# Kernel optimization log

Hardware: AMD Instinct MI355X
Metric: run time of the kernel (lower is better)

## Reference

```python
import jax, jax.numpy as jnp
import numpy as np

GROUP_SIZE = 128
LORA_SCALING = 32.0 / 16.0  # lora_alpha / r


def _unpack_rows(q):
    # q: int32 [n, m] -> uint4 values [n*8, m], 8 nibbles per int32 along axis 0
    shifts = (jnp.arange(8, dtype=jnp.int32) * 4)
    vals = (q[:, None, :] >> shifts[None, :, None]) & 0xF
    return vals.reshape(q.shape[0] * 8, q.shape[1])


def _unpack_cols(q):
    # q: int32 [g, m] -> uint4 values [g, m*8], 8 nibbles per int32 along axis 1
    shifts = (jnp.arange(8, dtype=jnp.int32) * 4)
    vals = (q[:, :, None] >> shifts[None, None, :]) & 0xF
    return vals.reshape(q.shape[0], q.shape[1] * 8)


def setup_inputs() -> dict:
    key = jax.random.key(0)
    ks = jax.random.split(key, 6)
    in_f, out_f, tokens, r = 4096, 11008, 64, 16
    g = in_f // GROUP_SIZE  # 32 groups
    x = jax.random.normal(ks[0], (tokens, in_f), dtype=jnp.float32)
    qweight = jax.random.randint(ks[1], (in_f // 8, out_f), jnp.iinfo(jnp.int32).min, jnp.iinfo(jnp.int32).max, dtype=jnp.int32)
    qzeros = jax.random.randint(ks[2], (g, out_f // 8), jnp.iinfo(jnp.int32).min, jnp.iinfo(jnp.int32).max, dtype=jnp.int32)
    scales = jax.random.uniform(ks[3], (g, out_f), dtype=jnp.float32) * 0.01 + 0.001
    lora_A = jax.random.normal(ks[4], (r, in_f), dtype=jnp.float32) * 0.02
    lora_B = jax.random.normal(ks[5], (out_f, r), dtype=jnp.float32) * 0.02
    return {"x": x, "qweight": qweight, "qzeros": qzeros, "scales": scales,
            "lora_A": lora_A, "lora_B": lora_B}


def reference(x, qweight, qzeros, scales, lora_A, lora_B):
    in_f = qweight.shape[0] * 8
    # --- GPTQ int4 dequant ---
    wq = _unpack_rows(qweight).astype(jnp.float32)          # [in, out]
    zeros = (_unpack_cols(qzeros) + 1).astype(jnp.float32)  # [groups, out] (GPTQ +1 offset)
    g_idx = jnp.arange(in_f) // GROUP_SIZE                  # [in]
    W = scales[g_idx] * (wq - zeros[g_idx])                 # [in, out]
    # base quantized matmul
    result = x @ W                                          # [tokens, out]
    # --- LoRA adapter (single active adapter, dropout=0, tmp_weight=1) ---
    lora_out = (x @ lora_A.T) @ lora_B.T                    # [tokens, out]
    return result + lora_out * LORA_SCALING
```

## Files before the change

kernel.cpp:

```cpp
#include <hip/hip_runtime.h>
#include <stdint.h>

#define TOKENS 64
#define IN_F   4096
#define OUT_F  11008
#define RANK   16
#define GS     128
#define NG     32
#define ZCOLS  (OUT_F / 8)
#define LORA_SCALE 2.0f

using short8  = __attribute__((ext_vector_type(8))) short;
using float4v = __attribute__((ext_vector_type(4))) float;

static __device__ inline uint16_t f2bf(float f, float* back) {
    uint32_t u = __float_as_uint(f);
    uint32_t r = (u + 0x7FFFu + ((u >> 16) & 1u)) >> 16;
    *back = __uint_as_float(r << 16);
    return (uint16_t)r;
}

static __device__ inline float dot4(float4 a, float4 b) {
    return a.x * b.x + a.y * b.y + a.z * b.z + a.w * b.w;
}

__global__ __launch_bounds__(256) void prep_kernel(
        const float* __restrict__ x,
        const float* __restrict__ loraA,
        uint4* __restrict__ xf4,
        float* __restrict__ xsumT,
        float* __restrict__ midTT) {
    __shared__ float redg[256];
    __shared__ float redm[4][16];
    const int t    = blockIdx.x;
    const int tid  = threadIdx.x;
    const int lane = tid & 63;
    const int wv   = tid >> 6;

    float4 xv[4];
    const float4* xp = (const float4*)(x + (size_t)t * IN_F + tid * 16);
    #pragma unroll
    for (int i = 0; i < 4; ++i) xv[i] = xp[i];

    union { uint16_t u[16]; uint4 q[2]; } ob;
    float s = 0.f;
    #pragma unroll
    for (int i = 0; i < 4; ++i) {
        float b;
        ob.u[i * 4 + 0] = f2bf(xv[i].x, &b); s += b;
        ob.u[i * 4 + 1] = f2bf(xv[i].y, &b); s += b;
        ob.u[i * 4 + 2] = f2bf(xv[i].z, &b); s += b;
        ob.u[i * 4 + 3] = f2bf(xv[i].w, &b); s += b;
    }
    {
        const int mm = t >> 4, nn = t & 15;
        const int kchunk = tid >> 1;
        #pragma unroll
        for (int i = 0; i < 2; ++i) {
            const int qd = (tid * 2 + i) & 3;
            xf4[(size_t)((mm * 128 + kchunk) * 64 + qd * 16 + nn)] = ob.q[i];
        }
    }
    redg[tid] = s;

    float pj[16];
    #pragma unroll
    for (int j = 0; j < 16; ++j) {
        const float4* ap = (const float4*)(loraA + (size_t)j * IN_F + tid * 16);
        float ps = 0.f;
        #pragma unroll
        for (int i = 0; i < 4; ++i) {
            float4 a = ap[i];
            ps += a.x * xv[i].x + a.y * xv[i].y + a.z * xv[i].z + a.w * xv[i].w;
        }
        pj[j] = ps;
    }
    #pragma unroll
    for (int j = 0; j < 16; ++j) {
        #pragma unroll
        for (int off = 32; off; off >>= 1) pj[j] += __shfl_down(pj[j], off);
    }
    if (lane == 0) {
        #pragma unroll
        for (int j = 0; j < 16; ++j) redm[wv][j] = pj[j];
    }
    __syncthreads();
    if (tid < NG) {
        float g = 0.f;
        #pragma unroll
        for (int i = 0; i < 8; ++i) g += redg[tid * 8 + i];
        xsumT[tid * TOKENS + t] = g;
    }
    if (tid < 16)
        midTT[t * RANK + tid] = redm[0][tid] + redm[1][tid] + redm[2][tid] + redm[3][tid];
}

#define LOADG(st, g) do {                                                       \
    _Pragma("unroll")                                                           \
    for (int mt = 0; mt < 2; ++mt)                                              \
        _Pragma("unroll")                                                       \
        for (int ks = 0; ks < 4; ++ks)                                          \
            A[st][mt * 4 + ks] =                                                \
                xf4[(size_t)(((mh * 2 + mt) * 128 + (g) * 4 + ks) * 64) + lane];\
    _Pragma("unroll")                                                           \
    for (int ks = 0; ks < 4; ++ks)                                              \
        B[st][ks] = qwc[(size_t)((g) * 16 + ks * 4 + quad) * OUT_F];            \
    _Pragma("unroll")                                                           \
    for (int mt = 0; mt < 2; ++mt)                                              \
        XS[st][mt] = *(const float4*)(xsumT + (g) * 64 +                        \
                                      (mh * 2 + mt) * 16 + quad * 4);           \
    S[st] = scales[(size_t)(g) * OUT_F + col];                                  \
    Z[st] = qz[(size_t)(g) * ZCOLS + (col >> 3)];                               \
} while (0)

#define COMPUTEG(st) do {                                                       \
    float4v accg[2];                                                            \
    accg[0] = (float4v){0.f, 0.f, 0.f, 0.f};                                    \
    accg[1] = (float4v){0.f, 0.f, 0.f, 0.f};                                    \
    _Pragma("unroll")                                                           \
    for (int ks = 0; ks < 4; ++ks) {                                            \
        union { uint4 u; short8 s; } af0, af1;                                  \
        af0.u = A[st][ks];                                                      \
        af1.u = A[st][4 + ks];                                                  \
        uint32_t q  = B[st][ks];                                                \
        uint32_t lo = q & 0x0F0F0F0Fu;                                          \
        uint32_t hi = (q >> 4) & 0x0F0F0F0Fu;                                   \
        union { uint32_t u32[4]; short8 s8; } bf;                               \
        _Pragma("unroll")                                                       \
        for (int i = 0; i < 4; ++i)                                             \
            bf.u32[i] = __builtin_amdgcn_perm(hi, lo,                           \
                            0x0C040C00u + i * 0x00010001u) | 0x43004300u;       \
        accg[0] = __builtin_amdgcn_mfma_f32_16x16x32_bf16(af0.s, bf.s8,         \
                                                          accg[0], 0, 0, 0);    \
        accg[1] = __builtin_amdgcn_mfma_f32_16x16x32_bf16(af1.s, bf.s8,         \
                                                          accg[1], 0, 0, 0);    \
    }                                                                           \
    {                                                                           \
        const float zoff = (float)(((Z[st] >> ((col & 7) * 4)) & 0xFu) + 129u); \
        const float scl = S[st];                                                \
        _Pragma("unroll")                                                       \
        for (int mt = 0; mt < 2; ++mt) {                                        \
            const float xr[4] = {XS[st][mt].x, XS[st][mt].y,                    \
                                 XS[st][mt].z, XS[st][mt].w};                   \
            _Pragma("unroll")                                                   \
            for (int r = 0; r < 4; ++r)                                         \
                acc[mt][r] = fmaf(scl, fmaf(-zoff, xr[r],                       \
                                  accg[mt][r]), acc[mt][r]);                    \
        }                                                                       \
    }                                                                           \
} while (0)

__global__ __launch_bounds__(256) void main_kernel(
        const uint32_t* __restrict__ qw,
        const uint32_t* __restrict__ qz,
        const float* __restrict__ scales,
        const uint4* __restrict__ xf4,
        const float* __restrict__ xsumT,
        const float* __restrict__ midTT,
        const float* __restrict__ loraB,
        float* __restrict__ out) {
    const int tid  = threadIdx.x;
    const int wv   = tid >> 6;
    const int lane = tid & 63;
    const int n    = lane & 15;
    const int quad = lane >> 4;
    const int mh   = wv & 1;
    const int cs   = wv >> 1;
    const int col  = blockIdx.x * 32 + cs * 16 + n;

    const uint32_t* qwc = qw + col;

    float4v acc[2];
    acc[0] = (float4v){0.f, 0.f, 0.f, 0.f};
    acc[1] = (float4v){0.f, 0.f, 0.f, 0.f};

    uint4    A[2][8];
    uint32_t B[2][4];
    float4   XS[2][2];
    float    S[2];
    uint32_t Z[2];

    LOADG(0, 0);
    LOADG(1, 1);
    #pragma unroll 2
    for (int g = 0; g < NG - 2; ++g) {
        const int st = g & 1;
        COMPUTEG(st);
        LOADG(st, g + 2);
    }
    COMPUTEG((NG - 2) & 1);
    COMPUTEG((NG - 1) & 1);

    const float4* b4 = (const float4*)(loraB + (size_t)col * RANK);
    const float4 b0 = b4[0], b1 = b4[1], b2 = b4[2], b3 = b4[3];
    #pragma unroll
    for (int mt = 0; mt < 2; ++mt) {
        #pragma unroll
        for (int r = 0; r < 4; ++r) {
            const int t = (mh * 2 + mt) * 16 + quad * 4 + r;
            const float4* m4 = (const float4*)(midTT + t * RANK);
            const float l = dot4(b0, m4[0]) + dot4(b1, m4[1]) +
                            dot4(b2, m4[2]) + dot4(b3, m4[3]);
            out[(size_t)t * OUT_F + col] = acc[mt][r] + LORA_SCALE * l;
        }
    }
}

extern "C" void kernel_launch(void* const* d_in, const int* in_sizes, int n_in,
                              void* d_out, int out_size, void* d_ws, size_t ws_size,
                              hipStream_t stream) {
    const float*    x      = (const float*)d_in[0];
    const uint32_t* qw     = (const uint32_t*)d_in[1];
    const uint32_t* qz     = (const uint32_t*)d_in[2];
    const float*    scales = (const float*)d_in[3];
    const float*    loraA  = (const float*)d_in[4];
    const float*    loraB  = (const float*)d_in[5];
    float* out = (float*)d_out;

    uint4* xf4   = (uint4*)d_ws;
    float* xsumT = (float*)((char*)d_ws + (size_t)TOKENS * IN_F * 2);
    float* midTT = xsumT + NG * TOKENS;

    prep_kernel<<<TOKENS, 256, 0, stream>>>(x, loraA, xf4, xsumT, midTT);
    main_kernel<<<OUT_F / 32, 256, 0, stream>>>(qw, qz, scales, xf4, xsumT,
                                                midTT, loraB, out);
}
```

Before: 113.4 us.

## Split the group loop across two wave halves with shared-memory reduction

```diff
diff --git a/kernel.cpp b/kernel.cpp
--- a/kernel.cpp
+++ b/kernel.cpp
@@ -150,7 +150,7 @@
     }                                                                           \
 } while (0)
 
-__global__ __launch_bounds__(256) void main_kernel(
+__global__ __launch_bounds__(512, 2) void main_kernel(
         const uint32_t* __restrict__ qw,
         const uint32_t* __restrict__ qz,
         const float* __restrict__ scales,
@@ -159,14 +159,17 @@
         const float* __restrict__ midTT,
         const float* __restrict__ loraB,
         float* __restrict__ out) {
+    __shared__ float red[4][64][8];
     const int tid  = threadIdx.x;
     const int wv   = tid >> 6;
     const int lane = tid & 63;
     const int n    = lane & 15;
     const int quad = lane >> 4;
-    const int mh   = wv & 1;
-    const int cs   = wv >> 1;
+    const int kh   = wv & 1;
+    const int mh   = (wv >> 1) & 1;
+    const int cs   = wv >> 2;
     const int col  = blockIdx.x * 32 + cs * 16 + n;
+    const int g0   = kh * 16;
 
     const uint32_t* qwc = qw + col;
 
@@ -180,28 +183,40 @@
     float    S[2];
     uint32_t Z[2];
 
-    LOADG(0, 0);
-    LOADG(1, 1);
+    LOADG(0, g0);
+    LOADG(1, g0 + 1);
     #pragma unroll 2
-    for (int g = 0; g < NG - 2; ++g) {
+    for (int g = 0; g < 14; ++g) {
         const int st = g & 1;
         COMPUTEG(st);
-        LOADG(st, g + 2);
-    }
-    COMPUTEG((NG - 2) & 1);
-    COMPUTEG((NG - 1) & 1);
-
-    const float4* b4 = (const float4*)(loraB + (size_t)col * RANK);
-    const float4 b0 = b4[0], b1 = b4[1], b2 = b4[2], b3 = b4[3];
-    #pragma unroll
-    for (int mt = 0; mt < 2; ++mt) {
-        #pragma unroll
-        for (int r = 0; r < 4; ++r) {
-            const int t = (mh * 2 + mt) * 16 + quad * 4 + r;
-            const float4* m4 = (const float4*)(midTT + t * RANK);
-            const float l = dot4(b0, m4[0]) + dot4(b1, m4[1]) +
-                            dot4(b2, m4[2]) + dot4(b3, m4[3]);
-            out[(size_t)t * OUT_F + col] = acc[mt][r] + LORA_SCALE * l;
+        LOADG(st, g0 + g + 2);
+    }
+    COMPUTEG(0);
+    COMPUTEG(1);
+
+    if (kh == 1) {
+        float* rp = &red[mh * 2 + cs][lane][0];
+        #pragma unroll
+        for (int mt = 0; mt < 2; ++mt)
+            #pragma unroll
+            for (int r = 0; r < 4; ++r) rp[mt * 4 + r] = acc[mt][r];
+    }
+    __syncthreads();
+    if (kh == 0) {
+        const float* rp = &red[mh * 2 + cs][lane][0];
+        const float4* b4 = (const float4*)(loraB + (size_t)col * RANK);
+        const float4 b0 = b4[0], b1 = b4[1], b2 = b4[2], b3 = b4[3];
+        #pragma unroll
+        for (int mt = 0; mt < 2; ++mt) {
+            #pragma unroll
+            for (int r = 0; r < 4; ++r) {
+                const int t = (mh * 2 + mt) * 16 + quad * 4 + r;
+                const float4* m4 = (const float4*)(midTT + t * RANK);
+                const float l = dot4(b0, m4[0]) + dot4(b1, m4[1]) +
+                                dot4(b2, m4[2]) + dot4(b3, m4[3]);
+                out[(size_t)t * OUT_F + col] =
+                    acc[mt][r] + rp[mt * 4 + r] + LORA_SCALE * l;
+            }
         }
     }
 }
@@ -222,6 +237,6 @@
     float* midTT = xsumT + NG * TOKENS;
 
     prep_kernel<<<TOKENS, 256, 0, stream>>>(x, loraA, xf4, xsumT, midTT);
-    main_kernel<<<OUT_F / 32, 256, 0, stream>>>(qw, qz, scales, xf4, xsumT,
+    main_kernel<<<OUT_F / 32, 512, 0, stream>>>(qw, qz, scales, xf4, xsumT,
                                                 midTT, loraB, out);
 }
```

Result: no change. 113.3 us (-0.1%).
